# Kernel optimization log

Measured on AMD Instinct MI355X. Metric: run time of the kernel, lower is better.

## Reference

```python
import jax, jax.numpy as jnp
import numpy as np

D_MODEL = 1024
NUM_HEADS = 16
D_K = D_MODEL // NUM_HEADS
SCALE = np.sqrt(D_K).astype(np.float32)


def setup_inputs() -> dict:
    key = jax.random.key(0)
    ks = jax.random.split(key, 11)
    B, S, D = 2, 2048, D_MODEL
    std = 1.0 / np.sqrt(D)
    inp = {
        "Q": jax.random.normal(ks[0], (B, S, D), dtype=jnp.float32),
        "K": jax.random.normal(ks[1], (B, S, D), dtype=jnp.float32),
        "V": jax.random.normal(ks[2], (B, S, D), dtype=jnp.float32),
        "Wq": jax.random.normal(ks[3], (D, D), dtype=jnp.float32) * std,
        "bq": jnp.zeros((D,), dtype=jnp.float32),
        "Wk": jax.random.normal(ks[4], (D, D), dtype=jnp.float32) * std,
        "bk": jnp.zeros((D,), dtype=jnp.float32),
        "Wv": jax.random.normal(ks[5], (D, D), dtype=jnp.float32) * std,
        "bv": jnp.zeros((D,), dtype=jnp.float32),
        "Wo": jax.random.normal(ks[6], (D, D), dtype=jnp.float32) * std,
        "bo": jnp.zeros((D,), dtype=jnp.float32),
    }
    return inp


def reference(Q, K, V, Wq, bq, Wk, bk, Wv, bv, Wo, bo):
    B, S, D = Q.shape
    H, dk = NUM_HEADS, D_K
    # Linear projections then split heads: [B, S, D] -> [B, H, S, dk]
    def proj(x, W, b):
        y = x @ W.T + b
        return y.reshape(B, -1, H, dk).transpose(0, 2, 1, 3)
    q = proj(Q, Wq, bq)
    k = proj(K, Wk, bk)
    v = proj(V, Wv, bv)
    # scores: [B, H, S, S]
    scores = jnp.einsum("bhqd,bhkd->bhqk", q, k) / SCALE
    attn = jax.nn.softmax(scores, axis=-1)
    # dropout is identity in eval mode
    context = jnp.einsum("bhqk,bhkd->bhqd", attn, v)
    context = context.transpose(0, 2, 1, 3).reshape(B, -1, D)
    output = context @ Wo.T + bo
    return output, attn
```

## Files before the change

kernel.cpp:

```cpp
#include <hip/hip_runtime.h>
#include <stdint.h>

#define BB 2
#define SS 2048
#define DD 1024
#define HH 16
#define DKK 64

typedef unsigned short u16;
typedef short short8 __attribute__((ext_vector_type(8)));
typedef float f32x4 __attribute__((ext_vector_type(4)));
typedef u16 u16x4 __attribute__((ext_vector_type(4)));

#define QSCALE 0.18033688011112042f

__device__ __forceinline__ u16 f2bf(float x){
  union { float f; uint32_t u; } v; v.f = x;
  uint32_t r = v.u + 0x7FFFu + ((v.u >> 16) & 1u);
  return (u16)(r >> 16);
}

struct ProjArgs {
  const void* A;
  const float* W;
  const float* bias;
  void* out;
  int mode;
  float oscale;
};

template<bool AF32>
__global__ __launch_bounds__(512)
void proj_kernel(ProjArgs a0, ProjArgs a1, ProjArgs a2)
{
  ProjArgs pa = (blockIdx.z == 0) ? a0 : (blockIdx.z == 1 ? a1 : a2);
  const int K = 1024;
  __shared__ __align__(16) u16 As[128*32];
  __shared__ __align__(16) u16 Bs[128*32];

  int tid = threadIdx.x;
  int wid = tid >> 6, lane = tid & 63;
  int lg = lane >> 4, lr = lane & 15;
  int tm = blockIdx.x * 128, tn = blockIdx.y * 128;
  int wr = (wid >> 2) * 64, wc = (wid & 3) * 32;

  const float* Af = (const float*)pa.A;
  const u16*   Ab = (const u16*)pa.A;
  const float* Wf = pa.W;

  f32x4 acc[4][2];
  #pragma unroll
  for (int m=0;m<4;m++)
    #pragma unroll
    for (int n=0;n<2;n++){ f32x4 z = {0.f,0.f,0.f,0.f}; acc[m][n] = z; }

  float4 raf[2], rbf[2];
  short8 rab;

  int s0 = tid,        r0 = s0 >> 3, c0 = (s0 & 7) * 4;
  int s1 = 512 + tid,  r1 = s1 >> 3, c1 = (s1 & 7) * 4;
  int rb_ = tid >> 2,  cb_ = (tid & 3) * 8;

  #define LOAD_TILE(kt)                                                        \
    do {                                                                       \
      if (AF32){                                                               \
        raf[0] = *(const float4*)(Af + (size_t)(tm + r0)*K + (kt) + c0);       \
        raf[1] = *(const float4*)(Af + (size_t)(tm + r1)*K + (kt) + c1);       \
      } else {                                                                 \
        rab = *(const short8*)(Ab + (size_t)(tm + rb_)*K + (kt) + cb_);        \
      }                                                                        \
      rbf[0] = *(const float4*)(Wf + (size_t)(tn + r0)*K + (kt) + c0);         \
      rbf[1] = *(const float4*)(Wf + (size_t)(tn + r1)*K + (kt) + c1);         \
    } while (0)

  LOAD_TILE(0);

  for (int kt = 0; kt < K; kt += 32){
    __syncthreads();
    if (AF32){
      u16x4 h0, h1;
      h0[0]=f2bf(raf[0].x); h0[1]=f2bf(raf[0].y); h0[2]=f2bf(raf[0].z); h0[3]=f2bf(raf[0].w);
      h1[0]=f2bf(raf[1].x); h1[1]=f2bf(raf[1].y); h1[2]=f2bf(raf[1].z); h1[3]=f2bf(raf[1].w);
      *(u16x4*)(As + r0*32 + c0) = h0;
      *(u16x4*)(As + r1*32 + c1) = h1;
    } else {
      *(short8*)(As + rb_*32 + cb_) = rab;
    }
    {
      u16x4 h0, h1;
      h0[0]=f2bf(rbf[0].x); h0[1]=f2bf(rbf[0].y); h0[2]=f2bf(rbf[0].z); h0[3]=f2bf(rbf[0].w);
      h1[0]=f2bf(rbf[1].x); h1[1]=f2bf(rbf[1].y); h1[2]=f2bf(rbf[1].z); h1[3]=f2bf(rbf[1].w);
      *(u16x4*)(Bs + r0*32 + c0) = h0;
      *(u16x4*)(Bs + r1*32 + c1) = h1;
    }
    __syncthreads();
    if (kt + 32 < K) LOAD_TILE(kt + 32);

    short8 af[4], bf[2];
    #pragma unroll
    for (int m=0;m<4;m++) af[m] = *(const short8*)(As + (wr + m*16 + lr)*32 + lg*8);
    #pragma unroll
    for (int n=0;n<2;n++) bf[n] = *(const short8*)(Bs + (wc + n*16 + lr)*32 + lg*8);
    #pragma unroll
    for (int m=0;m<4;m++)
      #pragma unroll
      for (int n=0;n<2;n++)
        acc[m][n] = __builtin_amdgcn_mfma_f32_16x16x32_bf16(af[m], bf[n], acc[m][n], 0,0,0);
  }
  #undef LOAD_TILE

  #pragma unroll
  for (int m=0;m<4;m++){
    #pragma unroll
    for (int n=0;n<2;n++){
      #pragma unroll
      for (int r=0;r<4;r++){
        int gm = tm + wr + m*16 + lg*4 + r;
        int gn = tn + wc + n*16 + lr;
        float v = (acc[m][n][r] + pa.bias[gn]) * pa.oscale;
        if (pa.mode == 3){
          ((float*)pa.out)[(size_t)gm*DD + gn] = v;
        } else {
          int b_ = gm >> 11, s_ = gm & 2047;
          int h_ = gn >> 6,  d_ = gn & 63;
          int bh = b_*HH + h_;
          u16 hv = f2bf(v);
          if (pa.mode == 0){
            ((u16*)pa.out)[((size_t)bh*SS + s_)*DKK + d_] = hv;
          } else if (pa.mode == 1){
            int c   = s_ >> 5;
            int lr2 = s_ & 15;
            int tl  = (s_ >> 4) & 1;
            int sub = tl*2 + (d_ >> 5);
            int lg2 = (d_ >> 3) & 3;
            int e   = d_ & 7;
            ((u16*)pa.out)[(((size_t)bh*64 + c)*4 + sub)*512 + (lg2*16 + lr2)*8 + e] = hv;
          } else {
            int c   = s_ >> 5;
            int lg2 = (s_ >> 3) & 3;
            int e   = s_ & 7;
            int dt  = d_ >> 4;
            int lr2 = d_ & 15;
            ((u16*)pa.out)[(((size_t)bh*64 + c)*4 + dt)*512 + (lg2*16 + lr2)*8 + e] = hv;
          }
        }
      }
    }
  }
}

__global__ __launch_bounds__(256, 3)
void attn_fused_kernel(const u16* __restrict__ qb, const u16* __restrict__ kf,
                       const u16* __restrict__ vf, float* __restrict__ attn_out,
                       u16* __restrict__ ctx)
{
  __shared__ __align__(16) u16 ptile[4][1280];
  __shared__ f32x4 accbuf[2][64][8];
  __shared__ float rsbuf[4][32];

  int tid = threadIdx.x;
  int w = tid >> 6, lane = tid & 63;
  int lg = lane >> 4, lr = lane & 15;
  int p = w >> 1, par = w & 1;
  int L  = blockIdx.x;
  int bh = (L & 7)*4 + ((L >> 3) & 3);
  int qg = ((L >> 5) << 1) + p;

  const u16* qp = qb + ((size_t)bh*SS + qg*32)*DKK;
  const u16* kp = kf + (size_t)bh*131072;
  const u16* vp = vf + (size_t)bh*131072;
  u16* myt = ptile[w];

  short8 qf[2][2];
  #pragma unroll
  for (int rt=0;rt<2;rt++){
    qf[rt][0] = *(const short8*)(qp + (rt*16+lr)*DKK + lg*8);
    qf[rt][1] = *(const short8*)(qp + (rt*16+lr)*DKK + 32 + lg*8);
  }

  f32x4 acc[2][4];
  #pragma unroll
  for (int rt=0;rt<2;rt++)
    #pragma unroll
    for (int dt=0;dt<4;dt++){ f32x4 z={0.f,0.f,0.f,0.f}; acc[rt][dt]=z; }
  float rsum[2] = {0.f, 0.f};

  short8 kc[4];
  #pragma unroll
  for (int s=0;s<4;s++)
    kc[s] = *(const short8*)(kp + ((size_t)par*4 + s)*512 + lane*8);

  for (int i=0;i<32;i++){
    int c = par + 2*i;
    short8 vc0 = *(const short8*)(vp + ((size_t)c*4 + 0)*512 + lane*8);
    short8 vc1 = *(const short8*)(vp + ((size_t)c*4 + 1)*512 + lane*8);
    short8 ka0=kc[0], ka1=kc[1], kb0=kc[2], kb1=kc[3];
    if (i < 31){
      #pragma unroll
      for (int s=0;s<4;s++)
        kc[s] = *(const short8*)(kp + ((size_t)(c+2)*4 + s)*512 + lane*8);
    }
    #pragma unroll
    for (int rt=0;rt<2;rt++){
      f32x4 sA = {0.f,0.f,0.f,0.f}, sB = {0.f,0.f,0.f,0.f};
      sA = __builtin_amdgcn_mfma_f32_16x16x32_bf16(ka0, qf[rt][0], sA, 0,0,0);
      sA = __builtin_amdgcn_mfma_f32_16x16x32_bf16(ka1, qf[rt][1], sA, 0,0,0);
      sB = __builtin_amdgcn_mfma_f32_16x16x32_bf16(kb0, qf[rt][0], sB, 0,0,0);
      sB = __builtin_amdgcn_mfma_f32_16x16x32_bf16(kb1, qf[rt][1], sB, 0,0,0);
      u16x4 hA, hB;
      #pragma unroll
      for (int r=0;r<4;r++){
        float pA = __builtin_exp2f(sA[r]);
        float pB = __builtin_exp2f(sB[r]);
        rsum[rt] += pA + pB;
        hA[r] = f2bf(pA);
        hB[r] = f2bf(pB);
      }
      *(u16x4*)(myt + (rt*16+lr)*40 + lg*4)      = hA;
      *(u16x4*)(myt + (rt*16+lr)*40 + 16 + lg*4) = hB;
    }
    short8 vc2 = *(const short8*)(vp + ((size_t)c*4 + 2)*512 + lane*8);
    short8 vc3 = *(const short8*)(vp + ((size_t)c*4 + 3)*512 + lane*8);
    #pragma unroll
    for (int rt=0;rt<2;rt++){
      short8 pa = *(const short8*)(myt + (rt*16+lr)*40 + lg*8);
      acc[rt][0] = __builtin_amdgcn_mfma_f32_16x16x32_bf16(pa, vc0, acc[rt][0], 0,0,0);
      acc[rt][1] = __builtin_amdgcn_mfma_f32_16x16x32_bf16(pa, vc1, acc[rt][1], 0,0,0);
      acc[rt][2] = __builtin_amdgcn_mfma_f32_16x16x32_bf16(pa, vc2, acc[rt][2], 0,0,0);
      acc[rt][3] = __builtin_amdgcn_mfma_f32_16x16x32_bf16(pa, vc3, acc[rt][3], 0,0,0);
    }
  }

  #pragma unroll
  for (int rt=0;rt<2;rt++){
    float v = rsum[rt];
    v += __shfl_xor(v, 16);
    v += __shfl_xor(v, 32);
    if (lg == 0) rsbuf[w][rt*16 + lr] = v;
  }
  if (par == 1){
    #pragma unroll
    for (int rt=0;rt<2;rt++)
      #pragma unroll
      for (int dt=0;dt<4;dt++)
        accbuf[p][lane][rt*4+dt] = acc[rt][dt];
  }
  __syncthreads();

  float il[2];
  #pragma unroll
  for (int rt=0;rt<2;rt++)
    il[rt] = 1.0f / (rsbuf[p*2][rt*16 + lr] + rsbuf[p*2+1][rt*16 + lr]);

  if (par == 0){
    int b_ = bh >> 4, h_ = bh & 15;
    #pragma unroll
    for (int rt=0;rt<2;rt++){
      #pragma unroll
      for (int dt=0;dt<4;dt++)
        acc[rt][dt] += accbuf[p][lane][rt*4+dt];
      #pragma unroll
      for (int r=0;r<4;r++){
        float ilr = __shfl(il[rt], lg*4 + r, 16);
        int row = qg*32 + rt*16 + lg*4 + r;
        #pragma unroll
        for (int dt=0;dt<4;dt++){
          float vv = acc[rt][dt][r] * ilr;
          ctx[((size_t)b_*SS + row)*DD + h_*DKK + dt*16 + lr] = f2bf(vv);
        }
      }
    }
  }

  #pragma unroll
  for (int s=0;s<4;s++)
    kc[s] = *(const short8*)(kp + ((size_t)par*4 + s)*512 + lane*8);
  float* arow0 = attn_out + ((size_t)bh*SS + qg*32 + lr)*SS;
  float* arow1 = attn_out + ((size_t)bh*SS + qg*32 + 16 + lr)*SS;
  for (int i=0;i<32;i++){
    int c = par + 2*i;
    short8 ka0=kc[0], ka1=kc[1], kb0=kc[2], kb1=kc[3];
    if (i < 31){
      #pragma unroll
      for (int s=0;s<4;s++)
        kc[s] = *(const short8*)(kp + ((size_t)(c+2)*4 + s)*512 + lane*8);
    }
    #pragma unroll
    for (int rt=0;rt<2;rt++){
      f32x4 sA = {0.f,0.f,0.f,0.f}, sB = {0.f,0.f,0.f,0.f};
      sA = __builtin_amdgcn_mfma_f32_16x16x32_bf16(ka0, qf[rt][0], sA, 0,0,0);
      sA = __builtin_amdgcn_mfma_f32_16x16x32_bf16(ka1, qf[rt][1], sA, 0,0,0);
      sB = __builtin_amdgcn_mfma_f32_16x16x32_bf16(kb0, qf[rt][0], sB, 0,0,0);
      sB = __builtin_amdgcn_mfma_f32_16x16x32_bf16(kb1, qf[rt][1], sB, 0,0,0);
      float myil = il[rt];
      f32x4 oA, oB;
      #pragma unroll
      for (int r=0;r<4;r++){
        oA[r] = __builtin_exp2f(sA[r]) * myil;
        oB[r] = __builtin_exp2f(sB[r]) * myil;
      }
      float* arow = (rt == 0) ? arow0 : arow1;
      *(f32x4*)(arow + c*32 + lg*4)      = oA;
      *(f32x4*)(arow + c*32 + 16 + lg*4) = oB;
    }
  }
}

extern "C" void kernel_launch(void* const* d_in, const int* in_sizes, int n_in,
                              void* d_out, int out_size, void* d_ws, size_t ws_size,
                              hipStream_t stream)
{
  const float* Q   = (const float*)d_in[0];
  const float* Kin = (const float*)d_in[1];
  const float* V   = (const float*)d_in[2];
  const float* Wq  = (const float*)d_in[3];
  const float* bq  = (const float*)d_in[4];
  const float* Wk  = (const float*)d_in[5];
  const float* bk  = (const float*)d_in[6];
  const float* Wv  = (const float*)d_in[7];
  const float* bv  = (const float*)d_in[8];
  const float* Wo  = (const float*)d_in[9];
  const float* bo  = (const float*)d_in[10];

  char* ws = (char*)d_ws;
  u16* qh  = (u16*)(ws + (size_t)( 0u<<20));
  u16* kfb = (u16*)(ws + (size_t)( 8u<<20));
  u16* vfb = (u16*)(ws + (size_t)(16u<<20));
  u16* ctx = (u16*)(ws + (size_t)(24u<<20));

  float* out0     = (float*)d_out;
  float* attn_out = out0 + (size_t)BB*SS*DD;

  ProjArgs pq = { Q,   Wq, bq, qh,   0, QSCALE };
  ProjArgs pk = { Kin, Wk, bk, kfb,  1, 1.0f   };
  ProjArgs pv = { V,   Wv, bv, vfb,  2, 1.0f   };
  ProjArgs po = { ctx, Wo, bo, out0, 3, 1.0f   };

  proj_kernel<true><<<dim3(32,8,3), 512, 0, stream>>>(pq, pk, pv);
  attn_fused_kernel<<<dim3(1024), 256, 0, stream>>>(qh, kfb, vfb, attn_out, ctx);
  proj_kernel<false><<<dim3(32,8,1), 512, 0, stream>>>(po, po, po);
}
```

Measured before the change: 293.0 us.

## Pre-convert inputs to bf16 and use direct global-to-LDS loads in projection GEMM

Adds a separate conversion kernel that turns Q, K, V and all four weight matrices into bf16 buffers in workspace. The projection GEMM then loads tiles with global_load_lds straight into shared memory, with no register staging or in-loop conversion. It also moves to 256 threads per block, each wave computing a 64x64 tile. The cost is an extra pass over the fp32 inputs (roughly 50MB read plus writes), and the register prefetch of the next tile is gone, so load latency is no longer overlapped with MFMA work.

```diff
diff --git a/kernel.cpp b/kernel.cpp
--- a/kernel.cpp
+++ b/kernel.cpp
@@ -20,17 +20,45 @@
   return (u16)(r >> 16);
 }
 
+typedef __attribute__((address_space(1))) const void gv_t;
+typedef __attribute__((address_space(3))) void lv_t;
+__device__ __forceinline__ void gload_lds16(const u16* g, u16* l){
+  __builtin_amdgcn_global_load_lds((gv_t*)g, (lv_t*)l, 16, 0, 0);
+}
+
+__global__ __launch_bounds__(256)
+void cvt_kernel(const float* __restrict__ a0, const float* __restrict__ a1,
+                const float* __restrict__ a2, const float* __restrict__ a3,
+                u16* __restrict__ o0, u16* __restrict__ o1,
+                u16* __restrict__ o2, u16* __restrict__ o3,
+                int n0, int n1, int n2, int n3)
+{
+  const float* a; u16* o; int n4;
+  switch (blockIdx.y) {
+    case 0:  a=a0; o=o0; n4=n0; break;
+    case 1:  a=a1; o=o1; n4=n1; break;
+    case 2:  a=a2; o=o2; n4=n2; break;
+    default: a=a3; o=o3; n4=n3; break;
+  }
+  int stride = gridDim.x * blockDim.x;
+  for (int i = blockIdx.x*blockDim.x + threadIdx.x; i < n4; i += stride){
+    float4 v = ((const float4*)a)[i];
+    u16x4 h;
+    h[0]=f2bf(v.x); h[1]=f2bf(v.y); h[2]=f2bf(v.z); h[3]=f2bf(v.w);
+    ((u16x4*)o)[i] = h;
+  }
+}
+
 struct ProjArgs {
-  const void* A;
-  const float* W;
+  const u16* A;
+  const u16* W;
   const float* bias;
   void* out;
   int mode;
   float oscale;
 };
 
-template<bool AF32>
-__global__ __launch_bounds__(512)
+__global__ __launch_bounds__(256)
 void proj_kernel(ProjArgs a0, ProjArgs a1, ProjArgs a2)
 {
   ProjArgs pa = (blockIdx.z == 0) ? a0 : (blockIdx.z == 1 ? a1 : a2);
@@ -42,77 +70,49 @@
   int wid = tid >> 6, lane = tid & 63;
   int lg = lane >> 4, lr = lane & 15;
   int tm = blockIdx.x * 128, tn = blockIdx.y * 128;
-  int wr = (wid >> 2) * 64, wc = (wid & 3) * 32;
-
-  const float* Af = (const float*)pa.A;
-  const u16*   Ab = (const u16*)pa.A;
-  const float* Wf = pa.W;
-
-  f32x4 acc[4][2];
+  int wr = (wid >> 1) * 64, wc = (wid & 1) * 64;
+
+  f32x4 acc[4][4];
   #pragma unroll
   for (int m=0;m<4;m++)
     #pragma unroll
-    for (int n=0;n<2;n++){ f32x4 z = {0.f,0.f,0.f,0.f}; acc[m][n] = z; }
-
-  float4 raf[2], rbf[2];
-  short8 rab;
-
-  int s0 = tid,        r0 = s0 >> 3, c0 = (s0 & 7) * 4;
-  int s1 = 512 + tid,  r1 = s1 >> 3, c1 = (s1 & 7) * 4;
-  int rb_ = tid >> 2,  cb_ = (tid & 3) * 8;
-
-  #define LOAD_TILE(kt)                                                        \
-    do {                                                                       \
-      if (AF32){                                                               \
-        raf[0] = *(const float4*)(Af + (size_t)(tm + r0)*K + (kt) + c0);       \
-        raf[1] = *(const float4*)(Af + (size_t)(tm + r1)*K + (kt) + c1);       \
-      } else {                                                                 \
-        rab = *(const short8*)(Ab + (size_t)(tm + rb_)*K + (kt) + cb_);        \
-      }                                                                        \
-      rbf[0] = *(const float4*)(Wf + (size_t)(tn + r0)*K + (kt) + c0);         \
-      rbf[1] = *(const float4*)(Wf + (size_t)(tn + r1)*K + (kt) + c1);         \
-    } while (0)
-
-  LOAD_TILE(0);
+    for (int n=0;n<4;n++){ f32x4 z = {0.f,0.f,0.f,0.f}; acc[m][n] = z; }
+
+  int sr = tid >> 2;
+  int sc = (tid & 3) * 8;
+  const u16* ga0 = pa.A + (size_t)(tm + sr)*K + sc;
+  const u16* ga1 = pa.A + (size_t)(tm + 64 + sr)*K + sc;
+  const u16* gb0 = pa.W + (size_t)(tn + sr)*K + sc;
+  const u16* gb1 = pa.W + (size_t)(tn + 64 + sr)*K + sc;
+  u16* la0 = As + sr*32 + sc;
+  u16* la1 = As + (64 + sr)*32 + sc;
+  u16* lb0 = Bs + sr*32 + sc;
+  u16* lb1 = Bs + (64 + sr)*32 + sc;
 
   for (int kt = 0; kt < K; kt += 32){
+    gload_lds16(ga0 + kt, la0);
+    gload_lds16(ga1 + kt, la1);
+    gload_lds16(gb0 + kt, lb0);
+    gload_lds16(gb1 + kt, lb1);
     __syncthreads();
-    if (AF32){
-      u16x4 h0, h1;
-      h0[0]=f2bf(raf[0].x); h0[1]=f2bf(raf[0].y); h0[2]=f2bf(raf[0].z); h0[3]=f2bf(raf[0].w);
-      h1[0]=f2bf(raf[1].x); h1[1]=f2bf(raf[1].y); h1[2]=f2bf(raf[1].z); h1[3]=f2bf(raf[1].w);
-      *(u16x4*)(As + r0*32 + c0) = h0;
-      *(u16x4*)(As + r1*32 + c1) = h1;
-    } else {
-      *(short8*)(As + rb_*32 + cb_) = rab;
-    }
-    {
-      u16x4 h0, h1;
-      h0[0]=f2bf(rbf[0].x); h0[1]=f2bf(rbf[0].y); h0[2]=f2bf(rbf[0].z); h0[3]=f2bf(rbf[0].w);
-      h1[0]=f2bf(rbf[1].x); h1[1]=f2bf(rbf[1].y); h1[2]=f2bf(rbf[1].z); h1[3]=f2bf(rbf[1].w);
-      *(u16x4*)(Bs + r0*32 + c0) = h0;
-      *(u16x4*)(Bs + r1*32 + c1) = h1;
-    }
+
+    short8 af[4], bf[4];
+    #pragma unroll
+    for (int m=0;m<4;m++) af[m] = *(const short8*)(As + (wr + m*16 + lr)*32 + lg*8);
+    #pragma unroll
+    for (int n=0;n<4;n++) bf[n] = *(const short8*)(Bs + (wc + n*16 + lr)*32 + lg*8);
+    #pragma unroll
+    for (int m=0;m<4;m++)
+      #pragma unroll
+      for (int n=0;n<4;n++)
+        acc[m][n] = __builtin_amdgcn_mfma_f32_16x16x32_bf16(af[m], bf[n], acc[m][n], 0,0,0);
     __syncthreads();
-    if (kt + 32 < K) LOAD_TILE(kt + 32);
-
-    short8 af[4], bf[2];
-    #pragma unroll
-    for (int m=0;m<4;m++) af[m] = *(const short8*)(As + (wr + m*16 + lr)*32 + lg*8);
-    #pragma unroll
-    for (int n=0;n<2;n++) bf[n] = *(const short8*)(Bs + (wc + n*16 + lr)*32 + lg*8);
-    #pragma unroll
-    for (int m=0;m<4;m++)
-      #pragma unroll
-      for (int n=0;n<2;n++)
-        acc[m][n] = __builtin_amdgcn_mfma_f32_16x16x32_bf16(af[m], bf[n], acc[m][n], 0,0,0);
-  }
-  #undef LOAD_TILE
+  }
 
   #pragma unroll
   for (int m=0;m<4;m++){
     #pragma unroll
-    for (int n=0;n<2;n++){
+    for (int n=0;n<4;n++){
       #pragma unroll
       for (int r=0;r<4;r++){
         int gm = tm + wr + m*16 + lg*4 + r;
@@ -323,20 +323,35 @@
   const float* bo  = (const float*)d_in[10];
 
   char* ws = (char*)d_ws;
-  u16* qh  = (u16*)(ws + (size_t)( 0u<<20));
-  u16* kfb = (u16*)(ws + (size_t)( 8u<<20));
-  u16* vfb = (u16*)(ws + (size_t)(16u<<20));
-  u16* ctx = (u16*)(ws + (size_t)(24u<<20));
+  u16* QB  = (u16*)(ws + (size_t)( 0u<<20));
+  u16* KB  = (u16*)(ws + (size_t)( 8u<<20));
+  u16* VB  = (u16*)(ws + (size_t)(16u<<20));
+  u16* WQB = (u16*)(ws + (size_t)(24u<<20));
+  u16* WKB = (u16*)(ws + (size_t)(26u<<20));
+  u16* WVB = (u16*)(ws + (size_t)(28u<<20));
+  u16* WOB = (u16*)(ws + (size_t)(30u<<20));
+  u16* qh  = (u16*)(ws + (size_t)(32u<<20));
+  u16* kfb = (u16*)(ws + (size_t)(40u<<20));
+  u16* vfb = (u16*)(ws + (size_t)(48u<<20));
+  u16* ctx = (u16*)(ws + (size_t)(56u<<20));
 
   float* out0     = (float*)d_out;
   float* attn_out = out0 + (size_t)BB*SS*DD;
 
-  ProjArgs pq = { Q,   Wq, bq, qh,   0, QSCALE };
-  ProjArgs pk = { Kin, Wk, bk, kfb,  1, 1.0f   };
-  ProjArgs pv = { V,   Wv, bv, vfb,  2, 1.0f   };
-  ProjArgs po = { ctx, Wo, bo, out0, 3, 1.0f   };
-
-  proj_kernel<true><<<dim3(32,8,3), 512, 0, stream>>>(pq, pk, pv);
+  int n_qkv = (BB*SS*DD)/4;
+  int n_w   = (DD*DD)/4;
+
+  cvt_kernel<<<dim3(512,4), 256, 0, stream>>>(Q, Kin, V, Wq, QB, KB, VB, WQB,
+                                              n_qkv, n_qkv, n_qkv, n_w);
+  cvt_kernel<<<dim3(256,3), 256, 0, stream>>>(Wk, Wv, Wo, Wo, WKB, WVB, WOB, WOB,
+                                              n_w, n_w, n_w, 0);
+
+  ProjArgs pq = { QB, WQB, bq, qh,   0, QSCALE };
+  ProjArgs pk = { KB, WKB, bk, kfb,  1, 1.0f   };
+  ProjArgs pv = { VB, WVB, bv, vfb,  2, 1.0f   };
+  ProjArgs po = { ctx, WOB, bo, out0, 3, 1.0f  };
+
+  proj_kernel<<<dim3(32,8,3), 256, 0, stream>>>(pq, pk, pv);
   attn_fused_kernel<<<dim3(1024), 256, 0, stream>>>(qh, kfb, vfb, attn_out, ctx);
-  proj_kernel<false><<<dim3(32,8,1), 512, 0, stream>>>(po, po, po);
-}
+  proj_kernel<<<dim3(32,8,1), 256, 0, stream>>>(po, po, po);
+}
```

After: 270.4 us. 1.08x faster.
